# Optimization experiments

Measured on AMD Instinct MI355X. Metric: run time of the kernel, lower is better.

The kernel has to match this reference:

```python
import jax, jax.numpy as jnp
import numpy as np

N_NODES = 100000
N_EDGES = 1600000
IN_C = 128
OUT_C = 64
NEG_SLOPE = 0.2  # PyG GATConv default
EPS = 1e-16      # PyG softmax denominator guard


def setup_inputs() -> dict:
    key = jax.random.key(0)
    k1, k2, k3, k4, k5, k6 = jax.random.split(key, 6)
    x = jax.random.normal(k1, (N_NODES, IN_C), dtype=jnp.float32)
    edge_index = jax.random.randint(k2, (2, N_EDGES), 0, N_NODES, dtype=jnp.int64)
    # Learned params (GATConv with heads=1): linear weight, attention vectors, bias
    W = jax.random.normal(k3, (IN_C, OUT_C), dtype=jnp.float32) * (1.0 / np.sqrt(IN_C))
    a_src = jax.random.normal(k4, (OUT_C,), dtype=jnp.float32) * (1.0 / np.sqrt(OUT_C))
    a_dst = jax.random.normal(k5, (OUT_C,), dtype=jnp.float32) * (1.0 / np.sqrt(OUT_C))
    b = jax.random.normal(k6, (OUT_C,), dtype=jnp.float32) * 0.01
    return {"x": x, "edge_index": edge_index, "W": W, "a_src": a_src, "a_dst": a_dst, "b": b}


def reference(x, edge_index, W, a_src, a_dst, b):
    N = x.shape[0]
    h = x @ W  # [N, OUT_C] transformed node features
    # add self loops (PyG default add_self_loops=True)
    loops = jnp.arange(N, dtype=edge_index.dtype)
    src = jnp.concatenate([edge_index[0], loops])  # [E+N]
    dst = jnp.concatenate([edge_index[1], loops])  # [E+N]
    # attention logits per edge: leaky_relu(a_src . h_src + a_dst . h_dst)
    s_src = h @ a_src  # [N]
    s_dst = h @ a_dst  # [N]
    logits = jax.nn.leaky_relu(s_src[src] + s_dst[dst], NEG_SLOPE)  # [E+N]
    # segment softmax over incoming edges of each destination node
    seg_max = jax.ops.segment_max(logits, dst, num_segments=N)  # [N]
    e = jnp.exp(logits - seg_max[dst])
    denom = jax.ops.segment_sum(e, dst, num_segments=N)  # [N]
    coef = e / (denom[dst] + EPS)  # [E+N]
    # weighted scatter-add of source messages
    out = jax.ops.segment_sum(coef[:, None] * h[src], dst, num_segments=N) + b  # [N, OUT_C]
    return jax.nn.elu(out)
```

## Files before the change

kernel.cpp:

```cpp
#include <hip/hip_runtime.h>
#include <math.h>

#define IN_C 128
#define OUT_C 64
#define NEG_SLOPE 0.2f
#define GAT_EPS 1e-16f

#define CSH 11
#define CN 2048
#define CAPC 36864
#define FSH 6
#define FN 64
#define FPC 32
#define CAPB 1536
#define RND 2048
#define SUBS 16
#define PACKS 20

typedef unsigned int uint;
typedef unsigned short ushort;

__device__ __forceinline__ ushort f2bf(float f) {
    uint u = __float_as_uint(f);
    return (ushort)((u + 0x7fffu + ((u >> 16) & 1u)) >> 16);
}

__global__ void zero_kernel(int* __restrict__ p, int n) {
    int i = blockIdx.x * blockDim.x + threadIdx.x;
    if (i < n) p[i] = 0;
}

__global__ __launch_bounds__(256) void gemm_kernel(
    const float* __restrict__ x, const float* __restrict__ W,
    const float* __restrict__ a_src, const float* __restrict__ a_dst,
    ushort* __restrict__ h16, float* __restrict__ s_src, float* __restrict__ s_dst,
    int N)
{
    __shared__ float Ws[IN_C * OUT_C];
    __shared__ float xs[64 * IN_C];
    const int t = threadIdx.x;

    {
        const float4* Wv = (const float4*)W;
        float4* Wsv = (float4*)Ws;
        #pragma unroll
        for (int i = 0; i < 8; i++) Wsv[t + i * 256] = Wv[t + i * 256];
    }
    const int row0 = blockIdx.x * 64;
    {
        #pragma unroll
        for (int i = 0; i < 8; i++) {
            int idx = t + i * 256;
            int r = idx >> 5;
            int kq = idx & 31;
            int row = row0 + r;
            float4 v = make_float4(0.f, 0.f, 0.f, 0.f);
            if (row < N) v = ((const float4*)(x + (size_t)row * IN_C))[kq];
            int sw = (r & 7) << 2;
            *(float4*)&xs[r * IN_C + ((kq * 4) ^ sw)] = v;
        }
    }
    __syncthreads();

    const int colq = t & 15;
    const int rg = t >> 4;
    float acc[4][4] = {};

    for (int kq = 0; kq < 32; kq++) {
        float4 xv[4];
        #pragma unroll
        for (int rr = 0; rr < 4; rr++) {
            int r = rg * 4 + rr;
            int sw = (r & 7) << 2;
            xv[rr] = *(const float4*)&xs[r * IN_C + ((kq * 4) ^ sw)];
        }
        #pragma unroll
        for (int j = 0; j < 4; j++) {
            float4 wv = *(const float4*)&Ws[(kq * 4 + j) * OUT_C + colq * 4];
            #pragma unroll
            for (int rr = 0; rr < 4; rr++) {
                float xvj = ((const float*)&xv[rr])[j];
                acc[rr][0] += xvj * wv.x;
                acc[rr][1] += xvj * wv.y;
                acc[rr][2] += xvj * wv.z;
                acc[rr][3] += xvj * wv.w;
            }
        }
    }

    float4 as = ((const float4*)a_src)[colq];
    float4 ad = ((const float4*)a_dst)[colq];
    #pragma unroll
    for (int rr = 0; rr < 4; rr++) {
        int row = row0 + rg * 4 + rr;
        if (row < N) {
            uint2 pk;
            pk.x = (uint)f2bf(acc[rr][0]) | ((uint)f2bf(acc[rr][1]) << 16);
            pk.y = (uint)f2bf(acc[rr][2]) | ((uint)f2bf(acc[rr][3]) << 16);
            *(uint2*)&h16[(size_t)row * OUT_C + colq * 4] = pk;
            float ps = acc[rr][0] * as.x + acc[rr][1] * as.y + acc[rr][2] * as.z + acc[rr][3] * as.w;
            float pd = acc[rr][0] * ad.x + acc[rr][1] * ad.y + acc[rr][2] * ad.z + acc[rr][3] * ad.w;
            ps += __shfl_xor(ps, 1);  pd += __shfl_xor(pd, 1);
            ps += __shfl_xor(ps, 2);  pd += __shfl_xor(pd, 2);
            ps += __shfl_xor(ps, 4);  pd += __shfl_xor(pd, 4);
            ps += __shfl_xor(ps, 8);  pd += __shfl_xor(pd, 8);
            if (colq == 0) { s_src[row] = ps; s_dst[row] = pd; }
        }
    }
}

__global__ __launch_bounds__(256) void partA_kernel(
    const int* __restrict__ src, const int* __restrict__ dst,
    int* __restrict__ ccurA, int* __restrict__ ebufA, int E, int NC)
{
    __shared__ int scnt[64], sofs[64], gbase[64], rbase[64];
    __shared__ int rbuf[RND];
    __shared__ int garr[RND];
    const int t = threadIdx.x;
    const int e0 = blockIdx.x * RND;
    int tot = E - e0; if (tot > RND) tot = RND;

    if (t < 64) scnt[t] = 0;
    __syncthreads();
    #pragma unroll
    for (int k = 0; k < RND / 256; k++) {
        int i = k * 256 + t;
        if (i < tot) atomicAdd(&scnt[dst[e0 + i] >> CSH], 1);
    }
    __syncthreads();
    if (t < 64) {
        int v = scnt[t];
        int incl = v;
        #pragma unroll
        for (int off = 1; off < 64; off <<= 1) {
            int u = __shfl_up(incl, off);
            if (t >= off) incl += u;
        }
        int excl = incl - v;
        rbase[t] = excl;
        sofs[t] = excl;
        if (t < NC && v > 0) gbase[t] = t * CAPC + atomicAdd(&ccurA[t], v);
    }
    __syncthreads();
    #pragma unroll
    for (int k = 0; k < RND / 256; k++) {
        int i = k * 256 + t;
        if (i < tot) {
            int d = dst[e0 + i];
            int c = d >> CSH;
            int q = atomicAdd(&sofs[c], 1);
            rbuf[q] = ((d & (CN - 1)) << PACKS) | src[e0 + i];
            int g = gbase[c] + (q - rbase[c]);
            garr[q] = (g < (c + 1) * CAPC) ? g : -1;
        }
    }
    __syncthreads();
    for (int i = t; i < tot; i += 256) {
        int g = garr[i];
        if (g >= 0) ebufA[g] = rbuf[i];
    }
}

__global__ __launch_bounds__(256) void partB_kernel(
    const int* __restrict__ ccurA, int* __restrict__ ccurB,
    const int* __restrict__ ebufA, int* __restrict__ ebufB, int NC)
{
    __shared__ int scnt[FPC], sofs[FPC], gbase[FPC], rbase[FPC];
    __shared__ int rbuf[RND];
    __shared__ int garr[RND];
    const int c = blockIdx.x / SUBS;
    const int sub = blockIdx.x % SUBS;
    if (c >= NC) return;
    const int t = threadIdx.x;
    int len = ccurA[c]; if (len > CAPC) len = CAPC;
    const int beg = c * CAPC;
    const int nrounds = (len + RND - 1) / RND;

    for (int r = sub; r < nrounds; r += SUBS) {
        const int e0 = beg + r * RND;
        int tot = beg + len - e0; if (tot > RND) tot = RND;
        if (t < FPC) scnt[t] = 0;
        __syncthreads();
        #pragma unroll
        for (int k = 0; k < RND / 256; k++) {
            int i = k * 256 + t;
            if (i < tot) atomicAdd(&scnt[(ebufA[e0 + i] >> (PACKS + FSH)) & (FPC - 1)], 1);
        }
        __syncthreads();
        if (t < FPC) {
            int v = scnt[t];
            int incl = v;
            #pragma unroll
            for (int off = 1; off < FPC; off <<= 1) {
                int u = __shfl_up(incl, off);
                if (t >= off) incl += u;
            }
            int excl = incl - v;
            rbase[t] = excl;
            sofs[t] = excl;
            int fg = c * FPC + t;
            if (v > 0) gbase[t] = fg * CAPB + atomicAdd(&ccurB[fg], v);
        }
        __syncthreads();
        #pragma unroll
        for (int k = 0; k < RND / 256; k++) {
            int i = k * 256 + t;
            if (i < tot) {
                int pk = ebufA[e0 + i];
                int f = (pk >> (PACKS + FSH)) & (FPC - 1);
                int q = atomicAdd(&sofs[f], 1);
                rbuf[q] = pk;
                int g = gbase[f] + (q - rbase[f]);
                garr[q] = (g < (c * FPC + f + 1) * CAPB) ? g : -1;
            }
        }
        __syncthreads();
        for (int i = t; i < tot; i += 256) {
            int g = garr[i];
            if (g >= 0) ebufB[g] = rbuf[i];
        }
        __syncthreads();
    }
}

__global__ __launch_bounds__(256) void nodeB_kernel(
    const int* __restrict__ ccurB, const int* __restrict__ ebufB,
    const float* __restrict__ s_src, const float* __restrict__ s_dst,
    const ushort* __restrict__ h16, const float* __restrict__ bias,
    float* __restrict__ out, int N)
{
    __shared__ int   csr_s[CAPB];
    __shared__ float csr_e[CAPB];
    __shared__ int lhist[FN], lofs[FN + 1], lcur[FN];

    const int b = blockIdx.x;
    const int t = threadIdx.x;
    const int node0 = b << FSH;
    const int nn = min(FN, N - node0);
    int cnt = ccurB[b]; if (cnt > CAPB) cnt = CAPB;
    const int base = b * CAPB;

    if (t < FN) lhist[t] = 0;
    __syncthreads();
    for (int i = t; i < cnt; i += 256)
        atomicAdd(&lhist[(ebufB[base + i] >> PACKS) & (FN - 1)], 1);
    __syncthreads();
    if (t < FN) {
        int v = lhist[t];
        int incl = v;
        #pragma unroll
        for (int off = 1; off < FN; off <<= 1) {
            int u = __shfl_up(incl, off);
            if (t >= off) incl += u;
        }
        lofs[t + 1] = incl;
        lcur[t] = incl - v;
        if (t == 0) lofs[0] = 0;
    }
    __syncthreads();
    for (int i = t; i < cnt; i += 256) {
        int pk = ebufB[base + i];
        int ld = (pk >> PACKS) & (FN - 1);
        int sj = pk & ((1 << PACKS) - 1);
        int q = atomicAdd(&lcur[ld], 1);
        float lg = s_src[sj] + s_dst[node0 + ld];
        lg = (lg > 0.f) ? lg : NEG_SLOPE * lg;
        csr_s[q] = sj;
        csr_e[q] = __expf(lg);
    }
    __syncthreads();

    const int w = t >> 6;
    const int l = t & 63;
    const int h2 = l >> 5;
    const int lp = l & 31;
    const float b0 = bias[2 * lp], b1 = bias[2 * lp + 1];

    for (int nl = w; nl < nn; nl += 4) {
        const int node = node0 + nl;
        const int jb = lofs[nl], je = lofs[nl + 1];
        float acc0 = 0.f, acc1 = 0.f, ds = 0.f;
        int j = jb + h2;
        for (; j + 6 < je; j += 8) {
            int s0 = csr_s[j],     s1 = csr_s[j + 2];
            int s2 = csr_s[j + 4], s3 = csr_s[j + 6];
            float e0 = csr_e[j],     e1 = csr_e[j + 2];
            float e2 = csr_e[j + 4], e3 = csr_e[j + 6];
            uint u0 = *(const uint*)&h16[(size_t)s0 * OUT_C + 2 * lp];
            uint u1 = *(const uint*)&h16[(size_t)s1 * OUT_C + 2 * lp];
            uint u2 = *(const uint*)&h16[(size_t)s2 * OUT_C + 2 * lp];
            uint u3 = *(const uint*)&h16[(size_t)s3 * OUT_C + 2 * lp];
            ds += (e0 + e1) + (e2 + e3);
            acc0 += e0 * __uint_as_float(u0 << 16) + e1 * __uint_as_float(u1 << 16)
                  + e2 * __uint_as_float(u2 << 16) + e3 * __uint_as_float(u3 << 16);
            acc1 += e0 * __uint_as_float(u0 & 0xffff0000u) + e1 * __uint_as_float(u1 & 0xffff0000u)
                  + e2 * __uint_as_float(u2 & 0xffff0000u) + e3 * __uint_as_float(u3 & 0xffff0000u);
        }
        for (; j < je; j += 2) {
            int sj = csr_s[j];
            float e = csr_e[j];
            uint u = *(const uint*)&h16[(size_t)sj * OUT_C + 2 * lp];
            ds += e;
            acc0 += e * __uint_as_float(u << 16);
            acc1 += e * __uint_as_float(u & 0xffff0000u);
        }
        acc0 += __shfl_xor(acc0, 32);
        acc1 += __shfl_xor(acc1, 32);
        ds   += __shfl_xor(ds, 32);

        float ls = s_src[node] + s_dst[node];
        ls = (ls > 0.f) ? ls : NEG_SLOPE * ls;
        float es = __expf(ls);
        uint us = *(const uint*)&h16[(size_t)node * OUT_C + 2 * lp];
        acc0 += es * __uint_as_float(us << 16);
        acc1 += es * __uint_as_float(us & 0xffff0000u);
        ds += es;

        float inv = 1.f / (ds + GAT_EPS);
        float v0 = acc0 * inv + b0;
        float v1 = acc1 * inv + b1;
        v0 = (v0 > 0.f) ? v0 : (__expf(v0) - 1.f);
        v1 = (v1 > 0.f) ? v1 : (__expf(v1) - 1.f);
        if (l < 32) *(float2*)&out[(size_t)node * OUT_C + 2 * lp] = make_float2(v0, v1);
    }
}

extern "C" void kernel_launch(void* const* d_in, const int* in_sizes, int n_in,
                              void* d_out, int out_size, void* d_ws, size_t ws_size,
                              hipStream_t stream)
{
    const float* x     = (const float*)d_in[0];
    const int*   ei    = (const int*)d_in[1];
    const float* W     = (const float*)d_in[2];
    const float* a_src = (const float*)d_in[3];
    const float* a_dst = (const float*)d_in[4];
    const float* b     = (const float*)d_in[5];
    float* out = (float*)d_out;

    const int N = in_sizes[0] / IN_C;
    const int E = in_sizes[1] / 2;
    const int NC = (N + CN - 1) >> CSH;
    const int NFB = (N + FN - 1) >> FSH;
    const int NFB_AL = NC * FPC;
    const int nroundsA = (E + RND - 1) / RND;
    const int GB = (N + 63) / 64;
    const int* src = ei;
    const int* dst = ei + E;

    ushort* h16    = (ushort*)d_ws;
    float* s_src_p = (float*)(h16 + (size_t)N * OUT_C);
    float* s_dst_p = s_src_p + N;
    int*   ccurA   = (int*)(s_dst_p + N);
    int*   ccurB   = ccurA + 64;
    int*   ebufB   = ccurB + NFB_AL;
    int*   ebufA   = (int*)d_out;

    zero_kernel<<<(64 + NFB_AL + 255) / 256, 256, 0, stream>>>(ccurA, 64 + NFB_AL);
    gemm_kernel<<<GB, 256, 0, stream>>>(x, W, a_src, a_dst, h16, s_src_p, s_dst_p, N);
    partA_kernel<<<nroundsA, 256, 0, stream>>>(src, dst, ccurA, ebufA, E, NC);
    partB_kernel<<<NC * SUBS, 256, 0, stream>>>(ccurA, ccurB, ebufA, ebufB, NC);
    nodeB_kernel<<<NFB, 256, 0, stream>>>(ccurB, ebufB, s_src_p, s_dst_p, h16, b, out, N);
}
```

Baseline: 223.1 us.

## Use bf16 MFMA for feature GEMM and fold zeroing into GEMM kernel

The fp32 FMA GEMM is replaced by bf16 MFMA 16x16x32 instructions. x and W are converted to bf16 as they are staged in shared memory, with a swizzled layout for the A operand and a pre-arranged layout for W. The separate zero_kernel launch is removed, and the GEMM blocks now clear the counter buffer instead. Converting x to bf16 lowers the precision of h and of the attention scores, and the h16 stores are now scalar 2-byte writes rather than packed ones.

```diff
diff --git a/kernel.cpp b/kernel.cpp
--- a/kernel.cpp
+++ b/kernel.cpp
@@ -19,92 +19,108 @@
 
 typedef unsigned int uint;
 typedef unsigned short ushort;
+typedef __attribute__((ext_vector_type(8))) short bf16x8;
+typedef __attribute__((ext_vector_type(4))) float f32x4;
 
 __device__ __forceinline__ ushort f2bf(float f) {
     uint u = __float_as_uint(f);
     return (ushort)((u + 0x7fffu + ((u >> 16) & 1u)) >> 16);
-}
-
-__global__ void zero_kernel(int* __restrict__ p, int n) {
-    int i = blockIdx.x * blockDim.x + threadIdx.x;
-    if (i < n) p[i] = 0;
 }
 
 __global__ __launch_bounds__(256) void gemm_kernel(
     const float* __restrict__ x, const float* __restrict__ W,
     const float* __restrict__ a_src, const float* __restrict__ a_dst,
     ushort* __restrict__ h16, float* __restrict__ s_src, float* __restrict__ s_dst,
-    int N)
-{
-    __shared__ float Ws[IN_C * OUT_C];
-    __shared__ float xs[64 * IN_C];
+    int N, int* __restrict__ zero_ptr, int zero_n)
+{
+    __shared__ __align__(16) ushort xs[64 * 128];
+    __shared__ __align__(16) ushort Wl[128 * 64];
     const int t = threadIdx.x;
 
     {
-        const float4* Wv = (const float4*)W;
-        float4* Wsv = (float4*)Ws;
-        #pragma unroll
-        for (int i = 0; i < 8; i++) Wsv[t + i * 256] = Wv[t + i * 256];
+        int zi = blockIdx.x * 256 + t;
+        if (zi < zero_n) zero_ptr[zi] = 0;
+    }
+
+    #pragma unroll
+    for (int q = 0; q < 8; q++) {
+        float4 wv = ((const float4*)W)[t * 8 + q];
+        #pragma unroll
+        for (int e = 0; e < 4; e++) {
+            int L = t * 32 + q * 4 + e;
+            int k = L >> 6, col = L & 63;
+            int kc = k >> 5, kg = (k >> 3) & 3, j = k & 7;
+            int ct = col >> 4, c16 = col & 15;
+            float v = (e == 0) ? wv.x : (e == 1) ? wv.y : (e == 2) ? wv.z : wv.w;
+            Wl[(((kc * 4 + ct) * 4 + kg) * 16 + c16) * 8 + j] = f2bf(v);
+        }
     }
     const int row0 = blockIdx.x * 64;
     {
-        #pragma unroll
-        for (int i = 0; i < 8; i++) {
-            int idx = t + i * 256;
-            int r = idx >> 5;
-            int kq = idx & 31;
-            int row = row0 + r;
-            float4 v = make_float4(0.f, 0.f, 0.f, 0.f);
-            if (row < N) v = ((const float4*)(x + (size_t)row * IN_C))[kq];
-            int sw = (r & 7) << 2;
-            *(float4*)&xs[r * IN_C + ((kq * 4) ^ sw)] = v;
-        }
-    }
-    __syncthreads();
-
-    const int colq = t & 15;
-    const int rg = t >> 4;
-    float acc[4][4] = {};
-
-    for (int kq = 0; kq < 32; kq++) {
-        float4 xv[4];
-        #pragma unroll
-        for (int rr = 0; rr < 4; rr++) {
-            int r = rg * 4 + rr;
-            int sw = (r & 7) << 2;
-            xv[rr] = *(const float4*)&xs[r * IN_C + ((kq * 4) ^ sw)];
-        }
-        #pragma unroll
-        for (int j = 0; j < 4; j++) {
-            float4 wv = *(const float4*)&Ws[(kq * 4 + j) * OUT_C + colq * 4];
+        int row_l = t >> 2;
+        int grow = row0 + row_l;
+        #pragma unroll
+        for (int qq = 0; qq < 4; qq++) {
+            int kq = (t & 3) * 4 + qq;
+            float4 v0 = make_float4(0.f, 0.f, 0.f, 0.f);
+            float4 v1 = v0;
+            if (grow < N) {
+                const float4* xp = (const float4*)(x + (size_t)grow * IN_C + kq * 8);
+                v0 = xp[0]; v1 = xp[1];
+            }
+            uint4 pk;
+            pk.x = (uint)f2bf(v0.x) | ((uint)f2bf(v0.y) << 16);
+            pk.y = (uint)f2bf(v0.z) | ((uint)f2bf(v0.w) << 16);
+            pk.z = (uint)f2bf(v1.x) | ((uint)f2bf(v1.y) << 16);
+            pk.w = (uint)f2bf(v1.z) | ((uint)f2bf(v1.w) << 16);
+            int slot = row_l * 16 + (kq ^ (row_l & 7));
+            *(uint4*)&xs[slot * 8] = pk;
+        }
+    }
+    __syncthreads();
+
+    const int wv_ = t >> 6;
+    const int l = t & 63;
+    const int c16 = l & 15;
+    const int quad = l >> 4;
+    const int row_a = wv_ * 16 + c16;
+
+    f32x4 acc[4] = {{0.f, 0.f, 0.f, 0.f}, {0.f, 0.f, 0.f, 0.f},
+                    {0.f, 0.f, 0.f, 0.f}, {0.f, 0.f, 0.f, 0.f}};
+
+    #pragma unroll
+    for (int kc = 0; kc < 4; kc++) {
+        int kq = kc * 4 + quad;
+        bf16x8 a = *(const bf16x8*)&xs[(row_a * 16 + (kq ^ (row_a & 7))) * 8];
+        #pragma unroll
+        for (int ct = 0; ct < 4; ct++) {
+            bf16x8 b = *(const bf16x8*)&Wl[(((kc * 4 + ct) * 4 + quad) * 16 + c16) * 8];
+            acc[ct] = __builtin_amdgcn_mfma_f32_16x16x32_bf16(a, b, acc[ct], 0, 0, 0);
+        }
+    }
+
+    float as4[4], ad4[4];
+    #pragma unroll
+    for (int ct = 0; ct < 4; ct++) {
+        as4[ct] = a_src[ct * 16 + c16];
+        ad4[ct] = a_dst[ct * 16 + c16];
+    }
+    #pragma unroll
+    for (int reg = 0; reg < 4; reg++) {
+        int row = row0 + wv_ * 16 + quad * 4 + reg;
+        float ps = acc[0][reg] * as4[0] + acc[1][reg] * as4[1]
+                 + acc[2][reg] * as4[2] + acc[3][reg] * as4[3];
+        float pd = acc[0][reg] * ad4[0] + acc[1][reg] * ad4[1]
+                 + acc[2][reg] * ad4[2] + acc[3][reg] * ad4[3];
+        ps += __shfl_xor(ps, 1);  pd += __shfl_xor(pd, 1);
+        ps += __shfl_xor(ps, 2);  pd += __shfl_xor(pd, 2);
+        ps += __shfl_xor(ps, 4);  pd += __shfl_xor(pd, 4);
+        ps += __shfl_xor(ps, 8);  pd += __shfl_xor(pd, 8);
+        if (row < N) {
             #pragma unroll
-            for (int rr = 0; rr < 4; rr++) {
-                float xvj = ((const float*)&xv[rr])[j];
-                acc[rr][0] += xvj * wv.x;
-                acc[rr][1] += xvj * wv.y;
-                acc[rr][2] += xvj * wv.z;
-                acc[rr][3] += xvj * wv.w;
-            }
-        }
-    }
-
-    float4 as = ((const float4*)a_src)[colq];
-    float4 ad = ((const float4*)a_dst)[colq];
-    #pragma unroll
-    for (int rr = 0; rr < 4; rr++) {
-        int row = row0 + rg * 4 + rr;
-        if (row < N) {
-            uint2 pk;
-            pk.x = (uint)f2bf(acc[rr][0]) | ((uint)f2bf(acc[rr][1]) << 16);
-            pk.y = (uint)f2bf(acc[rr][2]) | ((uint)f2bf(acc[rr][3]) << 16);
-            *(uint2*)&h16[(size_t)row * OUT_C + colq * 4] = pk;
-            float ps = acc[rr][0] * as.x + acc[rr][1] * as.y + acc[rr][2] * as.z + acc[rr][3] * as.w;
-            float pd = acc[rr][0] * ad.x + acc[rr][1] * ad.y + acc[rr][2] * ad.z + acc[rr][3] * ad.w;
-            ps += __shfl_xor(ps, 1);  pd += __shfl_xor(pd, 1);
-            ps += __shfl_xor(ps, 2);  pd += __shfl_xor(pd, 2);
-            ps += __shfl_xor(ps, 4);  pd += __shfl_xor(pd, 4);
-            ps += __shfl_xor(ps, 8);  pd += __shfl_xor(pd, 8);
-            if (colq == 0) { s_src[row] = ps; s_dst[row] = pd; }
+            for (int ct = 0; ct < 4; ct++)
+                h16[(size_t)row * OUT_C + ct * 16 + c16] = f2bf(acc[ct][reg]);
+            if (c16 == 0) { s_src[row] = ps; s_dst[row] = pd; }
         }
     }
 }
@@ -355,8 +371,8 @@
     int*   ebufB   = ccurB + NFB_AL;
     int*   ebufA   = (int*)d_out;
 
-    zero_kernel<<<(64 + NFB_AL + 255) / 256, 256, 0, stream>>>(ccurA, 64 + NFB_AL);
-    gemm_kernel<<<GB, 256, 0, stream>>>(x, W, a_src, a_dst, h16, s_src_p, s_dst_p, N);
+    gemm_kernel<<<GB, 256, 0, stream>>>(x, W, a_src, a_dst, h16, s_src_p, s_dst_p,
+                                        N, ccurA, 64 + NFB_AL);
     partA_kernel<<<nroundsA, 256, 0, stream>>>(src, dst, ccurA, ebufA, E, NC);
     partB_kernel<<<NC * SUBS, 256, 0, stream>>>(ccurA, ccurB, ebufA, ebufB, NC);
     nodeB_kernel<<<NFB, 256, 0, stream>>>(ccurB, ebufB, s_src_p, s_dst_p, h16, b, out, N);
```

New measurement: 204.0 us. 8.5% less time.
